# Kernel tuning notes

Measured on AMD Instinct MI355X. Metric: run time of the kernel, lower is better.

Reference implementation:

```python
import jax, jax.numpy as jnp
import numpy as np

B = 16384       # batch of Monte-Carlo paths
NSTEPS = 32     # time discretization N
H = 128         # hidden width of sub-networks
L = 1.0         # sphere radius l
T1 = 1.0
T0 = 0.0
DT = float((T1 - T0) / NSTEPS)


def _mlp(n, x, W1, b1, W2, b2):
    # sub-network on concat([N, X]): (B,1)+(B,3) -> (B,out)
    inp = jnp.concatenate([n, x], axis=-1)
    h = jnp.tanh(inp @ W1.T + b1)
    return h @ W2.T + b2


def _forward(process_N, process_X, discrete_t, delta_B,
             rW1, rb1, rW2, rb2, gW1, gb1, gW2, gb2, jW1, jb1, jW2, jb2):
    eye = jnp.eye(3, dtype=process_X.dtype)
    alpha = 0.3 * jax.nn.sigmoid(0.1 * process_N)    # birth intensity, (N+1,B,1)
    beta = 0.2 * jax.nn.sigmoid(-0.1 * process_N)    # death intensity, (N+1,B,1)
    u0 = _mlp(process_N[0], process_X[0], rW1, rb1, rW2, rb2)  # result net, (B,1)

    def step(u, xs):
        (Ni, Xi, Np1, ti, dB, ai, bi,
         gW1i, gb1i, gW2i, gb2i, jW1i, jb1i, jW2i, jb2i) = xs
        grad_u = _mlp(Ni, Xi, gW1i, gb1i, gW2i, gb2i)           # (B,3)
        outer = Xi[:, :, None] * Xi[:, None, :] / (L * L)       # (B,3,3)
        sigma = jnp.swapaxes(eye - outer, -2, -1)               # sigma0(X)^T
        T_inv = eye + outer
        k = jnp.sqrt(2.0 / (1.0 + 0.1 * Ni * Ni)) / L           # sqrt(2 D(N))/l, (B,1)
        kg = k * grad_u
        grad_bmm = jnp.einsum('bi,bij,bjk,bk->b', kg, T_inv, sigma, dB)[:, None]
        ui = _mlp(Ni, Xi, jW1i, jb1i, jW2i, jb2i)
        uip = _mlp(Ni + 1.0, Xi, jW1i, jb1i, jW2i, jb2i)
        uim = _mlp(Ni - 1.0, Xi, jW1i, jb1i, jW2i, jb2i)
        dp = uip - ui
        dm = uim - ui
        f = -0.05 * u + 0.05 * jnp.sum(grad_u * Xi, -1, keepdims=True) / L + 0.01 * ti
        u = u + grad_bmm - (ai * dp + bi * dm) * DT - f * DT
        dN = jnp.round(Np1 - Ni)
        u = u + jnp.where(dN > 0, dp, 0.0) + jnp.where(dN < 0, dm, 0.0)
        return u, None

    xs = (process_N[:-1], process_X[:-1], process_N[1:], discrete_t[:-1], delta_B,
          alpha[:-1], beta[:-1], gW1, gb1, gW2, gb2, jW1, jb1, jW2, jb2)
    u, _ = jax.lax.scan(step, u0, xs)
    g = 0.1 * process_N[-1] + jnp.cos(process_X[-1][:, :1])    # terminal condition
    return u, g


def setup_inputs():
    key = jax.random.key(0)
    ks = jax.random.split(key, 16)
    # integer-valued jump process N_t (kept float32), increments in {-1,0,1}
    n0 = jax.random.randint(ks[0], (1, B, 1), 5, 15).astype(jnp.float32)
    jumps = jax.random.randint(ks[1], (NSTEPS, B, 1), -1, 2).astype(jnp.float32)
    process_N = jnp.concatenate([n0, n0 + jnp.cumsum(jumps, axis=0)], axis=0)
    # spatial process on the sphere of radius L
    xr = jax.random.normal(ks[2], (NSTEPS + 1, B, 3), dtype=jnp.float32)
    process_X = L * xr / jnp.linalg.norm(xr, axis=-1, keepdims=True)
    discrete_t = jnp.linspace(T0, T1, NSTEPS + 1, dtype=jnp.float32)
    delta_B = jax.random.normal(ks[3], (NSTEPS, B, 3), dtype=jnp.float32) * float(np.sqrt(DT))

    def lin(k, shape, fan_in):
        return jax.random.normal(k, shape, dtype=jnp.float32) / float(np.sqrt(fan_in))

    rW1 = lin(ks[4], (H, 4), 4);           rb1 = jnp.zeros((H,), jnp.float32)
    rW2 = lin(ks[5], (1, H), H);           rb2 = jnp.zeros((1,), jnp.float32)
    gW1 = lin(ks[6], (NSTEPS, H, 4), 4);   gb1 = jnp.zeros((NSTEPS, H), jnp.float32)
    gW2 = lin(ks[7], (NSTEPS, 3, H), H);   gb2 = jnp.zeros((NSTEPS, 3), jnp.float32)
    jW1 = lin(ks[8], (NSTEPS, H, 4), 4);   jb1 = jnp.zeros((NSTEPS, H), jnp.float32)
    jW2 = lin(ks[9], (NSTEPS, 1, H), H);   jb2 = jnp.zeros((NSTEPS, 1), jnp.float32)
    return dict(process_N=process_N, process_X=process_X, discrete_t=discrete_t,
                delta_B=delta_B, rW1=rW1, rb1=rb1, rW2=rW2, rb2=rb2,
                gW1=gW1, gb1=gb1, gW2=gW2, gb2=gb2,
                jW1=jW1, jb1=jb1, jW2=jW2, jb2=jb2)


def reference(process_N, process_X, discrete_t, delta_B,
              rW1, rb1, rW2, rb2, gW1, gb1, gW2, gb2, jW1, jb1, jW2, jb2):
    return _forward(process_N, process_X, discrete_t, delta_B,
                    rW1, rb1, rW2, rb2, gW1, gb1, gW2, gb2, jW1, jb1, jW2, jb2)
```

## Files before the change

kernel.cpp:

```cpp
#include <hip/hip_runtime.h>
#include <math.h>

#define BB 16384
#define NSTEPS 32
#define HH 128
#define DTF (1.0f/32.0f)
#define SCALE 2.88539008177792681f
#define LOG2E 1.44269504088896340f

typedef float v2f __attribute__((ext_vector_type(2)));
typedef float v16f __attribute__((ext_vector_type(16)));
typedef unsigned int v2u __attribute__((ext_vector_type(2)));

#define SL(v,k) (__builtin_shufflevector((v),(v),2*(k),2*(k)+1))

__device__ __forceinline__ v2f pk_fma(v2f a, v2f b, v2f c) {
    return __builtin_elementwise_fma(a, b, c);
}

__device__ __forceinline__ v2f pk_rcp1(v2f x) {
    v2u xb; __builtin_memcpy(&xb, &x, 8);
    v2u yb = (v2u){0x7EF311C3u, 0x7EF311C3u} - xb;
    v2f y;  __builtin_memcpy(&y, &yb, 8);
    v2f u = pk_fma(-x, y, (v2f){2.0f, 2.0f});
    return y * u;
}

__device__ __forceinline__ float fexp2(float x) {
#if __has_builtin(__builtin_amdgcn_exp2f)
    return __builtin_amdgcn_exp2f(x);
#else
    float r; asm("v_exp_f32 %0, %1" : "=v"(r) : "v"(x)); return r;
#endif
}
__device__ __forceinline__ float frcp(float x) {
#if __has_builtin(__builtin_amdgcn_rcpf)
    return __builtin_amdgcn_rcpf(x);
#else
    float r; asm("v_rcp_f32 %0, %1" : "=v"(r) : "v"(x)); return r;
#endif
}
__device__ __forceinline__ float frsq(float x) {
#if __has_builtin(__builtin_amdgcn_rsqf)
    return __builtin_amdgcn_rsqf(x);
#else
    float r; asm("v_rsq_f32 %0, %1" : "=v"(r) : "v"(x)); return r;
#endif
}

__global__ __launch_bounds__(HH) void xform_kernel(
    const float* __restrict__ gW1, const float* __restrict__ gb1,
    const float* __restrict__ gW2, const float* __restrict__ gb2,
    const float* __restrict__ jW1, const float* __restrict__ jb1,
    const float* __restrict__ jW2,
    float* __restrict__ recA, float* __restrict__ G)
{
    const int i = blockIdx.x;
    const int j = threadIdx.x;
    const int pair = j >> 1;
    const int ln   = j & 1;
    float* r = recA + ((size_t)i*64 + pair)*32;

    const float* gw = gW1 + (size_t)(i*HH + j)*4;
    const float* jw = jW1 + (size_t)(i*HH + j)*4;
    float jw0 = jw[0];
    float g20 = gW2[i*3*HH + 0*HH + j];
    float g21 = gW2[i*3*HH + 1*HH + j];
    float g22 = gW2[i*3*HH + 2*HH + j];

    r[ 0+ln] = SCALE*gw[0];
    r[ 2+ln] = SCALE*gw[1];
    r[ 4+ln] = SCALE*gw[2];
    r[ 6+ln] = SCALE*gw[3];
    r[ 8+ln] = SCALE*gb1[i*HH + j];
    r[10+ln] = -2.0f*g20;
    r[12+ln] = -2.0f*g21;
    r[14+ln] = -2.0f*g22;

    r[16+ln] = SCALE*jw0;
    r[18+ln] = SCALE*jw[1];
    r[20+ln] = SCALE*jw[2];
    r[22+ln] = SCALE*jw[3];
    r[24+ln] = SCALE*jb1[i*HH + j];
    r[26+ln] = -2.0f*jW2[i*HH + j];
    r[28+ln] = exp2f( SCALE*jw0);
    r[30+ln] = exp2f(-SCALE*jw0);

    __shared__ float sh[3*HH];
    sh[0*HH + j] = g20; sh[1*HH + j] = g21; sh[2*HH + j] = g22;
    __syncthreads();
    if (j < 3) {
        float s = gb2[i*3 + j];
        for (int t = 0; t < HH; ++t) s += sh[j*HH + t];
        G[i*4 + j] = s;
    }
}

__global__ __launch_bounds__(256) void step_kernel(
    const float* __restrict__ N, const float* __restrict__ X,
    const float* __restrict__ T, const float* __restrict__ dB,
    const float* __restrict__ recA, const float* __restrict__ G,
    float* __restrict__ C)
{
    const int tid  = threadIdx.x;
    const int i    = blockIdx.x >> 8;
    const int bblk = blockIdx.x & 255;
    const int bl   = tid & 63;
    const int jq   = __builtin_amdgcn_readfirstlane(tid >> 6);
    const int b    = bblk*64 + bl;
    const int ib   = i*BB + b;

    const float Ni = N[ib];
    const float x0 = X[(size_t)ib*3 + 0], x1 = X[(size_t)ib*3 + 1], x2 = X[(size_t)ib*3 + 2];

    const v16f* rec16 = (const v16f*)(recA + (size_t)i*HH*16 + (size_t)jq*512);

    const v2f Niv  = {Ni, Ni};
    const v2f x0v  = {x0, x0};
    const v2f x1v  = {x1, x1};
    const v2f x2v  = {x2, x2};
    const v2f onev = {1.0f, 1.0f};
    const v2f c25v = {25.0f, 25.0f};

    v2f ga0 = {0.f,0.f}, ga1 = {0.f,0.f}, ga2 = {0.f,0.f};
    v2f a0  = {0.f,0.f}, aP  = {0.f,0.f}, aM  = {0.f,0.f};

#pragma unroll 2
    for (int t = 0; t < 16; ++t) {
        const v16f Rg = rec16[2*t + 0];
        const v16f Rj = rec16[2*t + 1];

        v2f ag = SL(Rg,4) * onev;
        ag = pk_fma(SL(Rg,0), Niv, ag);
        ag = pk_fma(SL(Rg,1), x0v, ag);
        ag = pk_fma(SL(Rg,2), x1v, ag);
        ag = pk_fma(SL(Rg,3), x2v, ag);
        ag = __builtin_elementwise_min(ag, c25v);
        v2f eg; eg.x = fexp2(ag.x); eg.y = fexp2(ag.y);
        v2f rg = pk_rcp1(eg + 1.0f);
        ga0 = pk_fma(SL(Rg,5), rg, ga0);
        ga1 = pk_fma(SL(Rg,6), rg, ga1);
        ga2 = pk_fma(SL(Rg,7), rg, ga2);

        v2f aj = SL(Rj,4) * onev;
        aj = pk_fma(SL(Rj,0), Niv, aj);
        aj = pk_fma(SL(Rj,1), x0v, aj);
        aj = pk_fma(SL(Rj,2), x1v, aj);
        aj = pk_fma(SL(Rj,3), x2v, aj);
        aj = __builtin_elementwise_min(aj, c25v);
        v2f ej; ej.x = fexp2(aj.x); ej.y = fexp2(aj.y);
        v2f r0 = pk_rcp1(ej + 1.0f);
        v2f rp = pk_rcp1(pk_fma(SL(Rj,6), ej, onev));
        v2f rm = pk_rcp1(pk_fma(SL(Rj,7), ej, onev));
        const v2f w2p = SL(Rj,5);
        a0 = pk_fma(w2p, r0, a0);
        aP = pk_fma(w2p, rp, aP);
        aM = pk_fma(w2p, rm, aM);
    }

    const float hga0 = ga0.x + ga0.y;
    const float hga1 = ga1.x + ga1.y;
    const float hga2 = ga2.x + ga2.y;
    const float ha0  = a0.x  + a0.y;
    const float haP  = aP.x  + aP.y;
    const float haM  = aM.x  + aM.y;

    __shared__ float sh[3][6][64];
    if (jq) {
        float* s = &sh[jq-1][0][bl];
        s[0*64] = hga0; s[1*64] = hga1; s[2*64] = hga2;
        s[3*64] = ha0;  s[4*64] = haP;  s[5*64] = haM;
    }
    __syncthreads();
    if (!jq) {
        float v0 = hga0, v1 = hga1, v2 = hga2;
        float v3 = ha0,  v4 = haP,  v5 = haM;
#pragma unroll
        for (int q = 0; q < 3; ++q) {
            v0 += sh[q][0][bl]; v1 += sh[q][1][bl]; v2 += sh[q][2][bl];
            v3 += sh[q][3][bl]; v4 += sh[q][4][bl]; v5 += sh[q][5][bl];
        }
        const float g0 = G[i*4 + 0] + v0;
        const float g1 = G[i*4 + 1] + v1;
        const float g2 = G[i*4 + 2] + v2;
        const float A0 = v3;
        const float AP = v4;
        const float AM = v5;

        const float Np1 = N[ib + BB];
        const float d0 = dB[(size_t)ib*3 + 0], d1 = dB[(size_t)ib*3 + 1], d2 = dB[(size_t)ib*3 + 2];
        const float ti = T[i];

        const float gdx = g0*x0 + g1*x1 + g2*x2;
        const float ss  = x0*x0 + x1*x1 + x2*x2;
        const float gdB = g0*d0 + g1*d1 + g2*d2;
        const float xdB = x0*d0 + x1*d1 + x2*d2;

        const float k = 1.41421356237309505f * frsq(fmaf(0.1f*Ni, Ni, 1.0f));
        const float grad_bmm = k * (gdB - ss*gdx*xdB);

        const float dp = AP - A0;
        const float dm = AM - A0;

        const float sig = frcp(1.0f + fexp2(-0.1f*LOG2E*Ni));
        const float alpha = 0.3f*sig;
        const float beta  = 0.2f - 0.2f*sig;

        const float dd = Np1 - Ni;
        const float jump = (dd > 0.5f) ? dp : ((dd < -0.5f) ? dm : 0.0f);

        const float c = grad_bmm - (alpha*dp + beta*dm)*DTF
                      - 0.05f*DTF*gdx - 0.01f*DTF*ti + jump;
        C[ib] = c;
    }
}

__global__ __launch_bounds__(256) void final_kernel(
    const float* __restrict__ N, const float* __restrict__ X,
    const float* __restrict__ rW1, const float* __restrict__ rb1,
    const float* __restrict__ rW2, const float* __restrict__ rb2,
    const float* __restrict__ C, float* __restrict__ out)
{
    const int gid = blockIdx.x*256 + threadIdx.x;
    const int b = gid >> 4;
    const int p = gid & 15;

    const float n0 = N[b];
    const float x0 = X[(size_t)b*3 + 0], x1 = X[(size_t)b*3 + 1], x2 = X[(size_t)b*3 + 2];

    float accw = 0.f, accr = 0.f;
#pragma unroll
    for (int t = 0; t < 8; ++t) {
        const int j = p*8 + t;
        float pre = fmaf(rW1[j*4+0], n0, fmaf(rW1[j*4+1], x0,
                    fmaf(rW1[j*4+2], x1, fmaf(rW1[j*4+3], x2, rb1[j]))));
        float r  = frcp(1.0f + fexp2(SCALE*pre));
        float w2 = rW2[j];
        accw += w2;
        accr = fmaf(w2, r, accr);
    }
    accw += __shfl_down(accw, 8, 16);  accr += __shfl_down(accr, 8, 16);
    accw += __shfl_down(accw, 4, 16);  accr += __shfl_down(accr, 4, 16);
    accw += __shfl_down(accw, 2, 16);  accr += __shfl_down(accr, 2, 16);
    accw += __shfl_down(accw, 1, 16);  accr += __shfl_down(accr, 1, 16);

    if (p == 0) {
        float u = rb2[0] + accw - 2.0f*accr;

        const float sfac = 1.0f + 0.05f*DTF;
#pragma unroll
        for (int i = 0; i < NSTEPS; ++i)
            u = fmaf(u, sfac, C[(size_t)i*BB + b]);
        out[b] = u;

        const int ib = NSTEPS*BB + b;
        out[BB + b] = fmaf(0.1f, N[ib], __cosf(X[(size_t)ib*3]));
    }
}

extern "C" void kernel_launch(void* const* d_in, const int* in_sizes, int n_in,
                              void* d_out, int out_size, void* d_ws, size_t ws_size,
                              hipStream_t stream)
{
    const float* N   = (const float*)d_in[0];
    const float* X   = (const float*)d_in[1];
    const float* T   = (const float*)d_in[2];
    const float* dB  = (const float*)d_in[3];
    const float* rW1 = (const float*)d_in[4];
    const float* rb1 = (const float*)d_in[5];
    const float* rW2 = (const float*)d_in[6];
    const float* rb2 = (const float*)d_in[7];
    const float* gW1 = (const float*)d_in[8];
    const float* gb1 = (const float*)d_in[9];
    const float* gW2 = (const float*)d_in[10];
    const float* gb2 = (const float*)d_in[11];
    const float* jW1 = (const float*)d_in[12];
    const float* jb1 = (const float*)d_in[13];
    const float* jW2 = (const float*)d_in[14];

    float* ws   = (float*)d_ws;
    float* C    = ws;
    float* recA = ws + (size_t)NSTEPS*BB;
    float* G    = recA + (size_t)NSTEPS*HH*16;
    float* out  = (float*)d_out;

    xform_kernel<<<NSTEPS, HH, 0, stream>>>(gW1, gb1, gW2, gb2, jW1, jb1, jW2, recA, G);
    step_kernel<<<NSTEPS*(BB/64), 256, 0, stream>>>(N, X, T, dB, recA, G, C);
    final_kernel<<<BB*16/256, 256, 0, stream>>>(N, X, rW1, rb1, rW2, rb2, C, out);
}
```

Baseline: 63.75 us.

## Move sigmoid reciprocals and second-layer dots to packed fp16

The step kernel's inner loop now converts the exp2 results to packed half precision. It computes the reciprocals with an fp16 bit-trick plus two Newton iterations and accumulates the second-layer weights with v_dot2_f32_f16, storing those weights as fp16 in the repacked record. The final kernel replaces the serial 32-step recurrence with a parallel weighted sum spread across the 16 lanes and a shuffle reduction. The xform bias sum becomes a tree reduction. The aim is fewer VALU ops per hidden unit, at the cost of fp16 rounding error in the MLP activations and outputs, with clamps at 10 and 16384 added to avoid overflow.

```diff
diff --git a/kernel.cpp b/kernel.cpp
--- a/kernel.cpp
+++ b/kernel.cpp
@@ -8,21 +8,32 @@
 #define SCALE 2.88539008177792681f
 #define LOG2E 1.44269504088896340f
 
-typedef float v2f __attribute__((ext_vector_type(2)));
+typedef float v2f  __attribute__((ext_vector_type(2)));
 typedef float v16f __attribute__((ext_vector_type(16)));
-typedef unsigned int v2u __attribute__((ext_vector_type(2)));
+typedef _Float16 h2 __attribute__((ext_vector_type(2)));
+typedef unsigned short u2s __attribute__((ext_vector_type(2)));
 
 #define SL(v,k) (__builtin_shufflevector((v),(v),2*(k),2*(k)+1))
 
 __device__ __forceinline__ v2f pk_fma(v2f a, v2f b, v2f c) {
     return __builtin_elementwise_fma(a, b, c);
 }
-
-__device__ __forceinline__ v2f pk_rcp1(v2f x) {
-    v2u xb; __builtin_memcpy(&xb, &x, 8);
-    v2u yb = (v2u){0x7EF311C3u, 0x7EF311C3u} - xb;
-    v2f y;  __builtin_memcpy(&y, &yb, 8);
-    v2f u = pk_fma(-x, y, (v2f){2.0f, 2.0f});
+__device__ __forceinline__ h2 h2fma(h2 a, h2 b, h2 c) {
+    return __builtin_elementwise_fma(a, b, c);
+}
+__device__ __forceinline__ h2 h2min(h2 a, h2 b) {
+    return __builtin_elementwise_min(a, b);
+}
+__device__ __forceinline__ h2 bch2(float f) { return __builtin_bit_cast(h2, f); }
+
+__device__ __forceinline__ h2 h2rcp2(h2 x) {
+    u2s xb = __builtin_bit_cast(u2s, x);
+    u2s yb = (u2s){(unsigned short)0x7799u, (unsigned short)0x7799u} - xb;
+    h2 y = __builtin_bit_cast(h2, yb);
+    const h2 two = {(_Float16)2.0f, (_Float16)2.0f};
+    h2 u = h2fma(-x, y, two);
+    y = y * u;
+    u = h2fma(-x, y, two);
     return y * u;
 }
 
@@ -46,6 +57,29 @@
 #else
     float r; asm("v_rsq_f32 %0, %1" : "=v"(r) : "v"(x)); return r;
 #endif
+}
+__device__ __forceinline__ h2 cvtpk(float a, float b) {
+    typedef __fp16 fh2 __attribute__((ext_vector_type(2)));
+#if __has_builtin(__builtin_amdgcn_cvt_pkrtz)
+    fh2 r = __builtin_amdgcn_cvt_pkrtz(a, b);
+    return __builtin_bit_cast(h2, r);
+#else
+    h2 r; r.x = (_Float16)a; r.y = (_Float16)b; return r;
+#endif
+}
+__device__ __forceinline__ float hdot2(h2 a, h2 b, float c) {
+    typedef __fp16 fh2 __attribute__((ext_vector_type(2)));
+#if __has_builtin(__builtin_amdgcn_fdot2)
+    return __builtin_amdgcn_fdot2(__builtin_bit_cast(fh2, a),
+                                  __builtin_bit_cast(fh2, b), c, false);
+#else
+    float d;
+    asm("v_dot2_f32_f16 %0, %1, %2, %3" : "=v"(d) : "v"(a), "v"(b), "v"(c));
+    return d;
+#endif
+}
+__device__ __forceinline__ unsigned short h16(float v) {
+    return __builtin_bit_cast(unsigned short, (_Float16)v);
 }
 
 __global__ __launch_bounds__(HH) void xform_kernel(
@@ -59,7 +93,8 @@
     const int j = threadIdx.x;
     const int pair = j >> 1;
     const int ln   = j & 1;
-    float* r = recA + ((size_t)i*64 + pair)*32;
+    float* r  = recA + ((size_t)i*64 + pair)*32;
+    float* rj = r + 16;
 
     const float* gw = gW1 + (size_t)(i*HH + j)*4;
     const float* jw = jW1 + (size_t)(i*HH + j)*4;
@@ -68,32 +103,34 @@
     float g21 = gW2[i*3*HH + 1*HH + j];
     float g22 = gW2[i*3*HH + 2*HH + j];
 
-    r[ 0+ln] = SCALE*gw[0];
-    r[ 2+ln] = SCALE*gw[1];
-    r[ 4+ln] = SCALE*gw[2];
-    r[ 6+ln] = SCALE*gw[3];
-    r[ 8+ln] = SCALE*gb1[i*HH + j];
-    r[10+ln] = -2.0f*g20;
-    r[12+ln] = -2.0f*g21;
-    r[14+ln] = -2.0f*g22;
-
-    r[16+ln] = SCALE*jw0;
-    r[18+ln] = SCALE*jw[1];
-    r[20+ln] = SCALE*jw[2];
-    r[22+ln] = SCALE*jw[3];
-    r[24+ln] = SCALE*jb1[i*HH + j];
-    r[26+ln] = -2.0f*jW2[i*HH + j];
-    r[28+ln] = exp2f( SCALE*jw0);
-    r[30+ln] = exp2f(-SCALE*jw0);
+    r[0+ln] = SCALE*gw[0]; r[2+ln] = SCALE*gw[1];
+    r[4+ln] = SCALE*gw[2]; r[6+ln] = SCALE*gw[3];
+    r[8+ln] = SCALE*gb1[i*HH + j];
+    ((unsigned short*)(r+10))[ln] = h16(-2.0f*g20);
+    ((unsigned short*)(r+11))[ln] = h16(-2.0f*g21);
+    ((unsigned short*)(r+12))[ln] = h16(-2.0f*g22);
+    r[13] = 0.f; r[14] = 0.f; r[15] = 0.f;
+
+    rj[0+ln] = SCALE*jw0;   rj[2+ln] = SCALE*jw[1];
+    rj[4+ln] = SCALE*jw[2]; rj[6+ln] = SCALE*jw[3];
+    rj[8+ln] = SCALE*jb1[i*HH + j];
+    ((unsigned short*)(rj+10))[ln] = h16(-2.0f*jW2[i*HH + j]);
+    ((unsigned short*)(rj+11))[ln] = h16(exp2f( SCALE*jw0));
+    ((unsigned short*)(rj+12))[ln] = h16(exp2f(-SCALE*jw0));
+    rj[13] = 0.f; rj[14] = 0.f; rj[15] = 0.f;
 
     __shared__ float sh[3*HH];
-    sh[0*HH + j] = g20; sh[1*HH + j] = g21; sh[2*HH + j] = g22;
+    sh[j] = g20; sh[HH + j] = g21; sh[2*HH + j] = g22;
     __syncthreads();
-    if (j < 3) {
-        float s = gb2[i*3 + j];
-        for (int t = 0; t < HH; ++t) s += sh[j*HH + t];
-        G[i*4 + j] = s;
-    }
+    for (int off = 64; off >= 1; off >>= 1) {
+        if (j < off) {
+            sh[j]      += sh[j + off];
+            sh[HH + j] += sh[HH + j + off];
+            sh[2*HH+j] += sh[2*HH + j + off];
+        }
+        __syncthreads();
+    }
+    if (j < 3) G[i*4 + j] = gb2[i*3 + j] + sh[j*HH];
 }
 
 __global__ __launch_bounds__(256) void step_kernel(
@@ -119,62 +156,56 @@
     const v2f x0v  = {x0, x0};
     const v2f x1v  = {x1, x1};
     const v2f x2v  = {x2, x2};
-    const v2f onev = {1.0f, 1.0f};
-    const v2f c25v = {25.0f, 25.0f};
-
-    v2f ga0 = {0.f,0.f}, ga1 = {0.f,0.f}, ga2 = {0.f,0.f};
-    v2f a0  = {0.f,0.f}, aP  = {0.f,0.f}, aM  = {0.f,0.f};
-
-#pragma unroll 2
+    const v2f c10v = {10.0f, 10.0f};
+    const h2  hone = {(_Float16)1.0f, (_Float16)1.0f};
+    const h2  c16k = {(_Float16)16384.0f, (_Float16)16384.0f};
+
+    float ga0 = 0.f, ga1 = 0.f, ga2 = 0.f;
+    float A0 = 0.f, AP = 0.f, AM = 0.f;
+
+#pragma unroll 4
     for (int t = 0; t < 16; ++t) {
         const v16f Rg = rec16[2*t + 0];
         const v16f Rj = rec16[2*t + 1];
 
-        v2f ag = SL(Rg,4) * onev;
+        v2f ag = SL(Rg,4);
         ag = pk_fma(SL(Rg,0), Niv, ag);
         ag = pk_fma(SL(Rg,1), x0v, ag);
         ag = pk_fma(SL(Rg,2), x1v, ag);
         ag = pk_fma(SL(Rg,3), x2v, ag);
-        ag = __builtin_elementwise_min(ag, c25v);
-        v2f eg; eg.x = fexp2(ag.x); eg.y = fexp2(ag.y);
-        v2f rg = pk_rcp1(eg + 1.0f);
-        ga0 = pk_fma(SL(Rg,5), rg, ga0);
-        ga1 = pk_fma(SL(Rg,6), rg, ga1);
-        ga2 = pk_fma(SL(Rg,7), rg, ga2);
-
-        v2f aj = SL(Rj,4) * onev;
+        ag = __builtin_elementwise_min(ag, c10v);
+        h2 eg = cvtpk(fexp2(ag.x), fexp2(ag.y));
+        h2 rg = h2rcp2(eg + hone);
+        ga0 = hdot2(bch2(Rg[10]), rg, ga0);
+        ga1 = hdot2(bch2(Rg[11]), rg, ga1);
+        ga2 = hdot2(bch2(Rg[12]), rg, ga2);
+
+        v2f aj = SL(Rj,4);
         aj = pk_fma(SL(Rj,0), Niv, aj);
         aj = pk_fma(SL(Rj,1), x0v, aj);
         aj = pk_fma(SL(Rj,2), x1v, aj);
         aj = pk_fma(SL(Rj,3), x2v, aj);
-        aj = __builtin_elementwise_min(aj, c25v);
-        v2f ej; ej.x = fexp2(aj.x); ej.y = fexp2(aj.y);
-        v2f r0 = pk_rcp1(ej + 1.0f);
-        v2f rp = pk_rcp1(pk_fma(SL(Rj,6), ej, onev));
-        v2f rm = pk_rcp1(pk_fma(SL(Rj,7), ej, onev));
-        const v2f w2p = SL(Rj,5);
-        a0 = pk_fma(w2p, r0, a0);
-        aP = pk_fma(w2p, rp, aP);
-        aM = pk_fma(w2p, rm, aM);
-    }
-
-    const float hga0 = ga0.x + ga0.y;
-    const float hga1 = ga1.x + ga1.y;
-    const float hga2 = ga2.x + ga2.y;
-    const float ha0  = a0.x  + a0.y;
-    const float haP  = aP.x  + aP.y;
-    const float haM  = aM.x  + aM.y;
+        aj = __builtin_elementwise_min(aj, c10v);
+        h2 ej = cvtpk(fexp2(aj.x), fexp2(aj.y));
+        h2 w2p = bch2(Rj[10]);
+        h2 r0 = h2rcp2(ej + hone);
+        h2 rp = h2rcp2(h2min(h2fma(ej, bch2(Rj[11]), hone), c16k));
+        h2 rm = h2rcp2(h2min(h2fma(ej, bch2(Rj[12]), hone), c16k));
+        A0 = hdot2(w2p, r0, A0);
+        AP = hdot2(w2p, rp, AP);
+        AM = hdot2(w2p, rm, AM);
+    }
 
     __shared__ float sh[3][6][64];
     if (jq) {
         float* s = &sh[jq-1][0][bl];
-        s[0*64] = hga0; s[1*64] = hga1; s[2*64] = hga2;
-        s[3*64] = ha0;  s[4*64] = haP;  s[5*64] = haM;
+        s[0*64] = ga0; s[1*64] = ga1; s[2*64] = ga2;
+        s[3*64] = A0;  s[4*64] = AP;  s[5*64] = AM;
     }
     __syncthreads();
     if (!jq) {
-        float v0 = hga0, v1 = hga1, v2 = hga2;
-        float v3 = ha0,  v4 = haP,  v5 = haM;
+        float v0 = ga0, v1 = ga1, v2 = ga2;
+        float v3 = A0,  v4 = AP,  v5 = AM;
 #pragma unroll
         for (int q = 0; q < 3; ++q) {
             v0 += sh[q][0][bl]; v1 += sh[q][1][bl]; v2 += sh[q][2][bl];
@@ -183,9 +214,6 @@
         const float g0 = G[i*4 + 0] + v0;
         const float g1 = G[i*4 + 1] + v1;
         const float g2 = G[i*4 + 2] + v2;
-        const float A0 = v3;
-        const float AP = v4;
-        const float AM = v5;
 
         const float Np1 = N[ib + BB];
         const float d0 = dB[(size_t)ib*3 + 0], d1 = dB[(size_t)ib*3 + 1], d2 = dB[(size_t)ib*3 + 2];
@@ -199,8 +227,8 @@
         const float k = 1.41421356237309505f * frsq(fmaf(0.1f*Ni, Ni, 1.0f));
         const float grad_bmm = k * (gdB - ss*gdx*xdB);
 
-        const float dp = AP - A0;
-        const float dm = AM - A0;
+        const float dp = v4 - v3;
+        const float dm = v5 - v3;
 
         const float sig = frcp(1.0f + fexp2(-0.1f*LOG2E*Ni));
         const float alpha = 0.3f*sig;
@@ -239,22 +267,24 @@
         accw += w2;
         accr = fmaf(w2, r, accr);
     }
-    accw += __shfl_down(accw, 8, 16);  accr += __shfl_down(accr, 8, 16);
-    accw += __shfl_down(accw, 4, 16);  accr += __shfl_down(accr, 4, 16);
-    accw += __shfl_down(accw, 2, 16);  accr += __shfl_down(accr, 2, 16);
-    accw += __shfl_down(accw, 1, 16);  accr += __shfl_down(accr, 1, 16);
+
+    const float l2s = 0.0022524617f;
+    const float wa = fexp2(l2s * (float)(31 - p));
+    const float wb = fexp2(l2s * (float)(15 - p));
+    float csum = fmaf(C[(size_t)p*BB + b], wa, C[(size_t)(p+16)*BB + b] * wb);
+
+    accw += __shfl_down(accw, 8, 16);  accr += __shfl_down(accr, 8, 16);  csum += __shfl_down(csum, 8, 16);
+    accw += __shfl_down(accw, 4, 16);  accr += __shfl_down(accr, 4, 16);  csum += __shfl_down(csum, 4, 16);
+    accw += __shfl_down(accw, 2, 16);  accr += __shfl_down(accr, 2, 16);  csum += __shfl_down(csum, 2, 16);
+    accw += __shfl_down(accw, 1, 16);  accr += __shfl_down(accr, 1, 16);  csum += __shfl_down(csum, 1, 16);
 
     if (p == 0) {
-        float u = rb2[0] + accw - 2.0f*accr;
-
-        const float sfac = 1.0f + 0.05f*DTF;
-#pragma unroll
-        for (int i = 0; i < NSTEPS; ++i)
-            u = fmaf(u, sfac, C[(size_t)i*BB + b]);
-        out[b] = u;
-
-        const int ib = NSTEPS*BB + b;
-        out[BB + b] = fmaf(0.1f, N[ib], __cosf(X[(size_t)ib*3]));
+        float u0 = rb2[0] + accw - 2.0f*accr;
+        const float s32 = 1.05123007f;
+        out[b] = fmaf(u0, s32, csum);
+
+        const int ibl = NSTEPS*BB + b;
+        out[BB + b] = fmaf(0.1f, N[ibl], __cosf(X[(size_t)ibl*3]));
     }
 }
 
```

Result: slower. 71.10 us (+11.5%).
